# Kernel tuning notes

Measured on AMD Instinct MI355X. Metric: run time of the kernel, lower is better.

## Reference

```python
import jax, jax.numpy as jnp
import numpy as np

D_LATENT = 2048
RANK = 16

def setup_inputs() -> dict:
    key = jax.random.key(0)
    k1, k2, k3 = jax.random.split(key, 3)
    h = jax.random.normal(k1, (4, 4096, D_LATENT), dtype=jnp.float32)
    # LoRA params: original init is randn/50 for A, zeros for B; use randn/50 for
    # both so the output is non-trivial for correctness testing.
    mat_A = jax.random.normal(k2, (D_LATENT, RANK), dtype=jnp.float32) / 50.0
    mat_B = jax.random.normal(k3, (RANK, D_LATENT), dtype=jnp.float32) / 50.0
    return {"h": h, "mat_A": mat_A, "mat_B": mat_B}

def reference(h, mat_A, mat_B):
    # Faithful to torch: F.linear(h, A @ B) == h @ (A @ B).T
    W = mat_A @ mat_B                      # [d_latent, d_latent]
    return jnp.einsum('bsd,ed->bse', h, W)  # h @ W.T
```

## Files before the change

### kernel.cpp

```cpp
#include <hip/hip_runtime.h>
#include <hip/hip_bf16.h>

typedef float f4 __attribute__((ext_vector_type(4)));
typedef short bf16x8 __attribute__((ext_vector_type(8)));

#define D 2048
#define RANK 16
#define NT 512

__device__ __forceinline__ short bf16_of(float x) {
    return __builtin_bit_cast(short, __float2bfloat16(x));
}

__device__ __forceinline__ bf16x8 cvt8(f4 lo, f4 hi) {
    bf16x8 r;
    r[0] = bf16_of(lo.x); r[1] = bf16_of(lo.y);
    r[2] = bf16_of(lo.z); r[3] = bf16_of(lo.w);
    r[4] = bf16_of(hi.x); r[5] = bf16_of(hi.y);
    r[6] = bf16_of(hi.z); r[7] = bf16_of(hi.w);
    return r;
}

__device__ __forceinline__ float dot4(f4 a, f4 b) {
    return a.x * b.x + a.y * b.y + a.z * b.z + a.w * b.w;
}

__device__ __forceinline__ void barrier_lgkm() {
    asm volatile("s_waitcnt lgkmcnt(0)" ::: "memory");
    __builtin_amdgcn_s_barrier();
}

__global__ __launch_bounds__(NT, 2)
void lora_pipe(const float* __restrict__ h, const float* __restrict__ A,
               const float* __restrict__ B, float* __restrict__ out) {
    const int tid  = threadIdx.x;
    const int wave = tid >> 6;
    const int lane = tid & 63;
    const int m16  = lane & 15;
    const int kg   = lane >> 4;
    const long row0 = (long)blockIdx.x * 32;

    __shared__ f4 ldsT[2][8][16][4];
    __shared__ f4 tt[2][16][4];

    const float* pB = B + (long)m16 * D + wave * 256 + kg * 8;
    bf16x8 Bb[8];
#pragma unroll
    for (int s = 0; s < 8; ++s) {
        f4 b0 = *(const f4*)(pB + s * 32);
        f4 b1 = *(const f4*)(pB + s * 32 + 4);
        Bb[s] = cvt8(b0, b1);
    }

    f4 Af[4][4];
#pragma unroll
    for (int j = 0; j < 4; ++j)
#pragma unroll
        for (int q = 0; q < 4; ++q)
            Af[j][q] = *(const f4*)(A + (long)(tid * 4 + j) * RANK + q * 4);

    const float* ph0 = h + (row0 + m16) * D + wave * 256 + kg * 8;

    f4 hc[16];
#pragma unroll
    for (int s = 0; s < 8; ++s) {
        hc[2 * s]     = *(const f4*)(ph0 + s * 32);
        hc[2 * s + 1] = *(const f4*)(ph0 + s * 32 + 4);
    }

    f4 a0 = {0.f, 0.f, 0.f, 0.f}, a1 = {0.f, 0.f, 0.f, 0.f};
#pragma unroll
    for (int s = 0; s < 4; ++s)
        a0 = __builtin_amdgcn_mfma_f32_16x16x32_bf16(
            Bb[s], cvt8(hc[2 * s], hc[2 * s + 1]), a0, 0, 0, 0);
#pragma unroll
    for (int s = 4; s < 8; ++s)
        a1 = __builtin_amdgcn_mfma_f32_16x16x32_bf16(
            Bb[s], cvt8(hc[2 * s], hc[2 * s + 1]), a1, 0, 0, 0);
    ldsT[0][wave][m16][kg] = a0 + a1;

    const float* ph1 = ph0 + 16 * D;
    f4 hn[16];
#pragma unroll
    for (int s = 0; s < 8; ++s) {
        hn[2 * s]     = *(const f4*)(ph1 + s * 32);
        hn[2 * s + 1] = *(const f4*)(ph1 + s * 32 + 4);
    }

    barrier_lgkm();
    if (tid < 64) {
        const int r = tid >> 2, q = tid & 3;
        f4 s = ldsT[0][0][r][q];
#pragma unroll
        for (int w = 1; w < 8; ++w) s += ldsT[0][w][r][q];
        tt[0][r][q] = s;
    }
    barrier_lgkm();

    a0 = (f4){0.f, 0.f, 0.f, 0.f};
    a1 = (f4){0.f, 0.f, 0.f, 0.f};
#pragma unroll
    for (int s = 0; s < 4; ++s)
        a0 = __builtin_amdgcn_mfma_f32_16x16x32_bf16(
            Bb[s], cvt8(hn[2 * s], hn[2 * s + 1]), a0, 0, 0, 0);
#pragma unroll
    for (int s = 4; s < 8; ++s)
        a1 = __builtin_amdgcn_mfma_f32_16x16x32_bf16(
            Bb[s], cvt8(hn[2 * s], hn[2 * s + 1]), a1, 0, 0, 0);
    ldsT[1][wave][m16][kg] = a0 + a1;

    {
        float* po = out + row0 * D + tid * 4;
#pragma unroll
        for (int r = 0; r < 16; ++r) {
            const f4 t0 = tt[0][r][0], t1 = tt[0][r][1];
            const f4 t2 = tt[0][r][2], t3 = tt[0][r][3];
            f4 res;
            res.x = dot4(t0, Af[0][0]) + dot4(t1, Af[0][1]) +
                    dot4(t2, Af[0][2]) + dot4(t3, Af[0][3]);
            res.y = dot4(t0, Af[1][0]) + dot4(t1, Af[1][1]) +
                    dot4(t2, Af[1][2]) + dot4(t3, Af[1][3]);
            res.z = dot4(t0, Af[2][0]) + dot4(t1, Af[2][1]) +
                    dot4(t2, Af[2][2]) + dot4(t3, Af[2][3]);
            res.w = dot4(t0, Af[3][0]) + dot4(t1, Af[3][1]) +
                    dot4(t2, Af[3][2]) + dot4(t3, Af[3][3]);
            __builtin_nontemporal_store(res, (f4*)(po + (long)r * D));
        }
    }

    barrier_lgkm();
    if (tid < 64) {
        const int r = tid >> 2, q = tid & 3;
        f4 s = ldsT[1][0][r][q];
#pragma unroll
        for (int w = 1; w < 8; ++w) s += ldsT[1][w][r][q];
        tt[1][r][q] = s;
    }
    barrier_lgkm();

    {
        float* po = out + (row0 + 16) * D + tid * 4;
#pragma unroll
        for (int r = 0; r < 16; ++r) {
            const f4 t0 = tt[1][r][0], t1 = tt[1][r][1];
            const f4 t2 = tt[1][r][2], t3 = tt[1][r][3];
            f4 res;
            res.x = dot4(t0, Af[0][0]) + dot4(t1, Af[0][1]) +
                    dot4(t2, Af[0][2]) + dot4(t3, Af[0][3]);
            res.y = dot4(t0, Af[1][0]) + dot4(t1, Af[1][1]) +
                    dot4(t2, Af[1][2]) + dot4(t3, Af[1][3]);
            res.z = dot4(t0, Af[2][0]) + dot4(t1, Af[2][1]) +
                    dot4(t2, Af[2][2]) + dot4(t3, Af[2][3]);
            res.w = dot4(t0, Af[3][0]) + dot4(t1, Af[3][1]) +
                    dot4(t2, Af[3][2]) + dot4(t3, Af[3][3]);
            __builtin_nontemporal_store(res, (f4*)(po + (long)r * D));
        }
    }
}

extern "C" void kernel_launch(void* const* d_in, const int* in_sizes, int n_in,
                              void* d_out, int out_size, void* d_ws,
                              size_t ws_size, hipStream_t stream) {
    const float* h = (const float*)d_in[0];
    const float* A = (const float*)d_in[1];
    const float* B = (const float*)d_in[2];
    float* out = (float*)d_out;

    const int n_rows = in_sizes[0] / D;
    const int blocks = n_rows / 32;

    hipLaunchKernelGGL(lora_pipe, dim3(blocks), dim3(NT), 0, stream,
                       h, A, B, out);
}
```

Baseline: 67.75 us.

## Convert LoRA kernel to persistent grid with register-prefetched 8-row tiles

Replaces the one-block-per-32-rows launch with a persistent grid of 256 blocks. Each block loops over 8-row tiles, prefetching the next tile of h into registers while the current tile's MFMAs and stores run, and keeps A and B resident in registers across iterations. The goal is to load and convert A/B once per block instead of per 32 rows, and to overlap global loads with compute. In exchange it drops to one block per CU with a single wave of blocks. Only 8 of the 16 MFMA rows carry useful data, so half the matrix work is wasted, and the launch assumes the row count divides evenly by 2048.

New measurement: 94.43 us. 39.4% more time.

```diff
diff --git a/kernel.cpp b/kernel.cpp
--- a/kernel.cpp
+++ b/kernel.cpp
@@ -6,7 +6,9 @@
 
 #define D 2048
 #define RANK 16
-#define NT 512
+#define NTHREADS 512
+#define GRID 256
+#define TROWS 8
 
 __device__ __forceinline__ short bf16_of(float x) {
     return __builtin_bit_cast(short, __float2bfloat16(x));
@@ -30,27 +32,19 @@
     __builtin_amdgcn_s_barrier();
 }
 
-__global__ __launch_bounds__(NT, 2)
-void lora_pipe(const float* __restrict__ h, const float* __restrict__ A,
-               const float* __restrict__ B, float* __restrict__ out) {
+__global__ __launch_bounds__(NTHREADS, 1)
+void lora_persist(const float* __restrict__ h, const float* __restrict__ A,
+                  const float* __restrict__ B, float* __restrict__ out,
+                  int iters) {
     const int tid  = threadIdx.x;
     const int wave = tid >> 6;
     const int lane = tid & 63;
     const int m16  = lane & 15;
     const int kg   = lane >> 4;
-    const long row0 = (long)blockIdx.x * 32;
+    const int bid  = blockIdx.x;
 
     __shared__ f4 ldsT[2][8][16][4];
-    __shared__ f4 tt[2][16][4];
-
-    const float* pB = B + (long)m16 * D + wave * 256 + kg * 8;
-    bf16x8 Bb[8];
-#pragma unroll
-    for (int s = 0; s < 8; ++s) {
-        f4 b0 = *(const f4*)(pB + s * 32);
-        f4 b1 = *(const f4*)(pB + s * 32 + 4);
-        Bb[s] = cvt8(b0, b1);
-    }
+    __shared__ f4 tt[2][8][4];
 
     f4 Af[4][4];
 #pragma unroll
@@ -59,62 +53,67 @@
         for (int q = 0; q < 4; ++q)
             Af[j][q] = *(const f4*)(A + (long)(tid * 4 + j) * RANK + q * 4);
 
-    const float* ph0 = h + (row0 + m16) * D + wave * 256 + kg * 8;
+    const float* pB = B + (long)m16 * D + wave * 256 + kg * 8;
+    bf16x8 Bb[8];
+#pragma unroll
+    for (int s = 0; s < 8; ++s)
+        Bb[s] = cvt8(*(const f4*)(pB + s * 32), *(const f4*)(pB + s * 32 + 4));
 
-    f4 hc[16];
+    const long hoff = (long)(m16 & 7) * D + wave * 256 + kg * 8;
+
+    f4 hf[16];
+    {
+        const float* ph = h + (long)bid * TROWS * D + hoff;
 #pragma unroll
-    for (int s = 0; s < 8; ++s) {
-        hc[2 * s]     = *(const f4*)(ph0 + s * 32);
-        hc[2 * s + 1] = *(const f4*)(ph0 + s * 32 + 4);
+        for (int s = 0; s < 8; ++s) {
+            hf[2 * s]     = *(const f4*)(ph + s * 32);
+            hf[2 * s + 1] = *(const f4*)(ph + s * 32 + 4);
+        }
     }
+    bf16x8 hb[8];
+#pragma unroll
+    for (int s = 0; s < 8; ++s) hb[s] = cvt8(hf[2 * s], hf[2 * s + 1]);
 
-    f4 a0 = {0.f, 0.f, 0.f, 0.f}, a1 = {0.f, 0.f, 0.f, 0.f};
+    for (int t = 0; t < iters; ++t) {
+        const int buf = t & 1;
+        const long tile = (long)t * GRID + bid;
+
+        if (t + 1 < iters) {
+            const float* pn =
+                h + ((long)(t + 1) * GRID + bid) * TROWS * D + hoff;
 #pragma unroll
-    for (int s = 0; s < 4; ++s)
-        a0 = __builtin_amdgcn_mfma_f32_16x16x32_bf16(
-            Bb[s], cvt8(hc[2 * s], hc[2 * s + 1]), a0, 0, 0, 0);
+            for (int s = 0; s < 8; ++s) {
+                hf[2 * s]     = *(const f4*)(pn + s * 32);
+                hf[2 * s + 1] = *(const f4*)(pn + s * 32 + 4);
+            }
+        }
+
+        f4 a0 = {0.f, 0.f, 0.f, 0.f}, a1 = {0.f, 0.f, 0.f, 0.f};
 #pragma unroll
-    for (int s = 4; s < 8; ++s)
-        a1 = __builtin_amdgcn_mfma_f32_16x16x32_bf16(
-            Bb[s], cvt8(hc[2 * s], hc[2 * s + 1]), a1, 0, 0, 0);
-    ldsT[0][wave][m16][kg] = a0 + a1;
+        for (int s = 0; s < 4; ++s)
+            a0 = __builtin_amdgcn_mfma_f32_16x16x32_bf16(Bb[s], hb[s], a0,
+                                                         0, 0, 0);
+#pragma unroll
+        for (int s = 4; s < 8; ++s)
+            a1 = __builtin_amdgcn_mfma_f32_16x16x32_bf16(Bb[s], hb[s], a1,
+                                                         0, 0, 0);
+        ldsT[buf][wave][m16][kg] = a0 + a1;
 
-    const float* ph1 = ph0 + 16 * D;
-    f4 hn[16];
+        barrier_lgkm();
+        if (tid < 32) {
+            const int r = tid >> 2, q = tid & 3;
+            f4 s = ldsT[buf][0][r][q];
 #pragma unroll
-    for (int s = 0; s < 8; ++s) {
-        hn[2 * s]     = *(const f4*)(ph1 + s * 32);
-        hn[2 * s + 1] = *(const f4*)(ph1 + s * 32 + 4);
-    }
+            for (int w = 1; w < 8; ++w) s += ldsT[buf][w][r][q];
+            tt[buf][r][q] = s;
+        }
+        barrier_lgkm();
 
-    barrier_lgkm();
-    if (tid < 64) {
-        const int r = tid >> 2, q = tid & 3;
-        f4 s = ldsT[0][0][r][q];
+        float* po = out + tile * TROWS * D + tid * 4;
 #pragma unroll
-        for (int w = 1; w < 8; ++w) s += ldsT[0][w][r][q];
-        tt[0][r][q] = s;
-    }
-    barrier_lgkm();
-
-    a0 = (f4){0.f, 0.f, 0.f, 0.f};
-    a1 = (f4){0.f, 0.f, 0.f, 0.f};
-#pragma unroll
-    for (int s = 0; s < 4; ++s)
-        a0 = __builtin_amdgcn_mfma_f32_16x16x32_bf16(
-            Bb[s], cvt8(hn[2 * s], hn[2 * s + 1]), a0, 0, 0, 0);
-#pragma unroll
-    for (int s = 4; s < 8; ++s)
-        a1 = __builtin_amdgcn_mfma_f32_16x16x32_bf16(
-            Bb[s], cvt8(hn[2 * s], hn[2 * s + 1]), a1, 0, 0, 0);
-    ldsT[1][wave][m16][kg] = a0 + a1;
-
-    {
-        float* po = out + row0 * D + tid * 4;
-#pragma unroll
-        for (int r = 0; r < 16; ++r) {
-            const f4 t0 = tt[0][r][0], t1 = tt[0][r][1];
-            const f4 t2 = tt[0][r][2], t3 = tt[0][r][3];
+        for (int r = 0; r < TROWS; ++r) {
+            const f4 t0 = tt[buf][r][0], t1 = tt[buf][r][1];
+            const f4 t2 = tt[buf][r][2], t3 = tt[buf][r][3];
             f4 res;
             res.x = dot4(t0, Af[0][0]) + dot4(t1, Af[0][1]) +
                     dot4(t2, Af[0][2]) + dot4(t3, Af[0][3]);
@@ -126,35 +125,20 @@
                     dot4(t2, Af[3][2]) + dot4(t3, Af[3][3]);
             __builtin_nontemporal_store(res, (f4*)(po + (long)r * D));
         }
-    }
 
-    barrier_lgkm();
-    if (tid < 64) {
-        const int r = tid >> 2, q = tid & 3;
-        f4 s = ldsT[1][0][r][q];
+        if (t + 1 < iters) {
 #pragma unroll
-        for (int w = 1; w < 8; ++w) s += ldsT[1][w][r][q];
-        tt[1][r][q] = s;
-    }
-    barrier_lgkm();
+            for (int s = 0; s < 8; ++s) hb[s] = cvt8(hf[2 * s], hf[2 * s + 1]);
+        }
 
-    {
-        float* po = out + (row0 + 16) * D + tid * 4;
-#pragma unroll
-        for (int r = 0; r < 16; ++r) {
-            const f4 t0 = tt[1][r][0], t1 = tt[1][r][1];
-            const f4 t2 = tt[1][r][2], t3 = tt[1][r][3];
-            f4 res;
-            res.x = dot4(t0, Af[0][0]) + dot4(t1, Af[0][1]) +
-                    dot4(t2, Af[0][2]) + dot4(t3, Af[0][3]);
-            res.y = dot4(t0, Af[1][0]) + dot4(t1, Af[1][1]) +
-                    dot4(t2, Af[1][2]) + dot4(t3, Af[1][3]);
-            res.z = dot4(t0, Af[2][0]) + dot4(t1, Af[2][1]) +
-                    dot4(t2, Af[2][2]) + dot4(t3, Af[2][3]);
-            res.w = dot4(t0, Af[3][0]) + dot4(t1, Af[3][1]) +
-                    dot4(t2, Af[3][2]) + dot4(t3, Af[3][3]);
-            __builtin_nontemporal_store(res, (f4*)(po + (long)r * D));
-        }
+        asm volatile("" : "+v"(Bb[0]), "+v"(Bb[1]), "+v"(Bb[2]), "+v"(Bb[3]),
+                          "+v"(Bb[4]), "+v"(Bb[5]), "+v"(Bb[6]), "+v"(Bb[7]));
+        asm volatile("" : "+v"(Af[0][0]), "+v"(Af[0][1]), "+v"(Af[0][2]),
+                          "+v"(Af[0][3]), "+v"(Af[1][0]), "+v"(Af[1][1]),
+                          "+v"(Af[1][2]), "+v"(Af[1][3]), "+v"(Af[2][0]),
+                          "+v"(Af[2][1]), "+v"(Af[2][2]), "+v"(Af[2][3]),
+                          "+v"(Af[3][0]), "+v"(Af[3][1]), "+v"(Af[3][2]),
+                          "+v"(Af[3][3]));
     }
 }
 
@@ -167,8 +151,8 @@
     float* out = (float*)d_out;
 
     const int n_rows = in_sizes[0] / D;
-    const int blocks = n_rows / 32;
+    const int iters  = n_rows / (GRID * TROWS);
 
-    hipLaunchKernelGGL(lora_pipe, dim3(blocks), dim3(NT), 0, stream,
-                       h, A, B, out);
+    hipLaunchKernelGGL(lora_persist, dim3(GRID), dim3(NTHREADS), 0, stream,
+                       h, A, B, out, iters);
 }
```
